# Optimization experiments

Measured on AMD Instinct MI355X. Metric: run time of the kernel, lower is better.

## Reference

```python
import jax, jax.numpy as jnp
import numpy as np

E = 384          # config.n_embd
H = 2 * E        # bidirectional hidden dim
B = 8
T = 128
L = 9            # num_labels


def _lstm_dir(x, w_ih, w_hh, b_ih, b_hh, reverse):
    # x: [B, T, D] -> outputs [B, T, E]
    xs = jnp.swapaxes(x, 0, 1)  # [T, B, D]
    if reverse:
        xs = xs[::-1]
    Eh = w_hh.shape[-1]
    h0 = jnp.zeros((x.shape[0], Eh), x.dtype)

    def step(carry, xt):
        h, c = carry
        g = xt @ w_ih.T + h @ w_hh.T + b_ih + b_hh
        i, f, gg, o = jnp.split(g, 4, axis=-1)
        i = jax.nn.sigmoid(i); f = jax.nn.sigmoid(f)
        gg = jnp.tanh(gg); o = jax.nn.sigmoid(o)
        c = f * c + i * gg
        h = o * jnp.tanh(c)
        return (h, c), h

    _, hs = jax.lax.scan(step, (h0, h0), xs)
    if reverse:
        hs = hs[::-1]
    return jnp.swapaxes(hs, 0, 1)


def bilstm(x, w_ih_l0, w_ih_rest, w_hh, b_ih, b_hh):
    # 3-layer bidirectional LSTM (eval mode: dropout off)
    h = x
    for l in range(3):
        wih = w_ih_l0 if l == 0 else w_ih_rest[l - 1]
        fw = _lstm_dir(h, wih[0], w_hh[l, 0], b_ih[l, 0], b_hh[l, 0], False)
        bw = _lstm_dir(h, wih[1], w_hh[l, 1], b_ih[l, 1], b_hh[l, 1], True)
        h = jnp.concatenate([fw, bw], axis=-1)
    return h  # [B, T, 2E]


def pos_attention(hs, query_ids, W_H, W_p, W_h, v):
    # Vectorized form of the original python loop over target positions.
    shared = hs @ W_H.T                                         # [B,Ts,H] (computed ONCE)
    h_p = jnp.take_along_axis(hs, query_ids[:, :, None].astype(jnp.int32)
                              .repeat(1, axis=1), axis=1)[:, 0, :]  # [B,H]
    p_term = h_p @ W_p.T                                        # [B,H]
    t_term = hs @ W_h.T                                         # [B,Tt,H]
    # score[b,t,s] = v . tanh(shared[b,s] + p_term[b] + t_term[b,t])
    z = jnp.tanh(shared[:, None, :, :] + (p_term[:, None, :] + t_term)[:, :, None, :])
    scores = jnp.einsum('btsh,h->bts', z, v[0])                 # [B,Tt,Ts]
    a = jax.nn.softmax(scores, axis=2)                          # softmax over source dim
    c = jnp.einsum('bts,bsh->bth', a, hs)                       # context [B,Tt,H]
    u = jnp.concatenate([hs, c], axis=-1)                       # [B,Tt,2H]
    at_pool = jnp.mean(a, axis=1)                               # [B,Ts]
    norm = at_pool / jnp.sum(at_pool, axis=1, keepdims=True)
    norm = jnp.nan_to_num(norm, nan=0.0)
    return norm, u


def viterbi_decode(emissions, trans, start, end):
    # emissions: [B,T,L] -> best tag path [B,T]
    score0 = start + emissions[:, 0]                            # [B,L]
    emis_rest = jnp.swapaxes(emissions, 0, 1)[1:]               # [T-1,B,L]

    def step(score, emis_t):
        cand = score[:, :, None] + trans[None]                  # [B,L,L]
        best = jnp.max(cand, axis=1) + emis_t
        ptr = jnp.argmax(cand, axis=1)                          # [B,L]
        return best, ptr

    final, ptrs = jax.lax.scan(step, score0, emis_rest)
    final = final + end
    last = jnp.argmax(final, axis=1)                            # [B]

    def back(tag, ptr_t):
        prev = jnp.take_along_axis(ptr_t, tag[:, None], axis=1)[:, 0]
        return prev, prev

    _, earlier = jax.lax.scan(back, last, ptrs[::-1])           # [T-1,B]
    tags = jnp.concatenate([earlier[::-1], last[None]], axis=0) # [T,B]
    return jnp.swapaxes(tags, 0, 1)                             # [B,T]


def setup_inputs() -> dict:
    key = jax.random.key(0)
    ks = jax.random.split(key, 16)
    s = 0.05
    inp = {}
    inp['input_embeds'] = jax.random.normal(ks[0], (B, T, E), jnp.float32)
    inp['query_ids'] = jax.random.randint(ks[1], (B, 1), 0, T)
    inp['w_ih_l0'] = jax.random.normal(ks[2], (2, 4 * E, E), jnp.float32) * s
    inp['w_ih_rest'] = jax.random.normal(ks[3], (2, 2, 4 * E, 2 * E), jnp.float32) * s
    inp['w_hh'] = jax.random.normal(ks[4], (3, 2, 4 * E, E), jnp.float32) * s
    inp['b_ih'] = jax.random.normal(ks[5], (3, 2, 4 * E), jnp.float32) * s
    inp['b_hh'] = jax.random.normal(ks[6], (3, 2, 4 * E), jnp.float32) * s
    inp['W_H'] = jax.random.normal(ks[7], (H, H), jnp.float32) * s
    inp['W_p'] = jax.random.normal(ks[8], (H, H), jnp.float32) * s
    inp['W_h'] = jax.random.normal(ks[9], (H, H), jnp.float32) * s
    inp['v'] = jax.random.normal(ks[10], (1, H), jnp.float32) * s
    inp['W_clf'] = jax.random.normal(ks[11], (L, 2 * H), jnp.float32) * s
    inp['crf_trans'] = jax.random.normal(ks[12], (L, L), jnp.float32) * s
    inp['crf_start'] = jax.random.normal(ks[13], (L,), jnp.float32) * s
    inp['crf_end'] = jax.random.normal(ks[14], (L,), jnp.float32) * s
    return inp


def reference(input_embeds, query_ids, w_ih_l0, w_ih_rest, w_hh, b_ih, b_hh,
              W_H, W_p, W_h, v, W_clf, crf_trans, crf_start, crf_end):
    hidden_states = bilstm(input_embeds, w_ih_l0, w_ih_rest, w_hh, b_ih, b_hh)
    a_t, u = pos_attention(hidden_states, query_ids, W_H, W_p, W_h, v)
    logits = u @ W_clf.T                                        # [B,T,L]
    tags = viterbi_decode(logits, crf_trans, crf_start, crf_end)
    vit_logits = jnp.where(tags[:, :, None] == jnp.arange(L)[None, None, :], 10, -1).astype(jnp.int8)
    return (vit_logits, hidden_states, a_t)
```

## Files before the change

### kernel.cpp

```cpp
#include <hip/hip_runtime.h>
#include <math.h>

#define Bq 8
#define Tt 128
#define Ee 384
#define Hh 768
#define Ll 9
#define GATE 1536

__device__ __forceinline__ float fast_sigmoid(float x) {
    return 1.f / (1.f + __expf(-x));
}
__device__ __forceinline__ float fast_tanh(float x) {
    return 1.f - 2.f / (__expf(2.f * x) + 1.f);
}

#define BM 64
#define BN 64
#define BKk 16

__global__ __launch_bounds__(256) void k_gemm(
    const float* __restrict__ A, const float* __restrict__ Bw, float* __restrict__ C,
    int M, int N, int K,
    long sAz, long sBz, long sCz,
    const float* __restrict__ b1, const float* __restrict__ b2, long sbz,
    const float* __restrict__ bbn)
{
    int z = blockIdx.z;
    A += (long)z * sAz;
    Bw += (long)z * sBz;
    C += (long)z * sCz;
    const float* bb1 = b1 ? b1 + (long)z * sbz : nullptr;
    const float* bb2 = b2 ? b2 + (long)z * sbz : nullptr;

    int n0 = blockIdx.x * BN;
    int m0 = blockIdx.y * BM;
    int tid = threadIdx.x;

    __shared__ float As[BKk][BM];
    __shared__ float Bs[BKk][BN];

    int lr = tid & 63;
    int lc = (tid >> 6) * 4;
    int tx = tid & 15;
    int ty = tid >> 4;

    float acc[4][4];
#pragma unroll
    for (int i = 0; i < 4; ++i)
#pragma unroll
        for (int j = 0; j < 4; ++j) acc[i][j] = 0.f;

    for (int k0 = 0; k0 < K; k0 += BKk) {
        float4 a0 = *(const float4*)&A[(long)(m0 + lr) * K + k0 + lc];
        float4 w0 = *(const float4*)&Bw[(long)(n0 + lr) * K + k0 + lc];
        __syncthreads();
        As[lc + 0][lr] = a0.x; As[lc + 1][lr] = a0.y; As[lc + 2][lr] = a0.z; As[lc + 3][lr] = a0.w;
        Bs[lc + 0][lr] = w0.x; Bs[lc + 1][lr] = w0.y; Bs[lc + 2][lr] = w0.z; Bs[lc + 3][lr] = w0.w;
        __syncthreads();
#pragma unroll
        for (int kk = 0; kk < BKk; ++kk) {
            float av[4], bv[4];
            *(float4*)&av[0] = *(float4*)&As[kk][ty * 4];
            *(float4*)&bv[0] = *(float4*)&Bs[kk][tx * 4];
#pragma unroll
            for (int i = 0; i < 4; ++i)
#pragma unroll
                for (int j = 0; j < 4; ++j)
                    acc[i][j] = fmaf(av[i], bv[j], acc[i][j]);
        }
    }

#pragma unroll
    for (int i = 0; i < 4; ++i) {
        long m = m0 + ty * 4 + i;
#pragma unroll
        for (int j = 0; j < 4; ++j) {
            int n = n0 + tx * 4 + j;
            float val = acc[i][j];
            if (bb1) val += bb1[n];
            if (bb2) val += bb2[n];
            if (bbn) val += bbn[(m >> 7) * (long)N + n];
            C[m * N + n] = val;
        }
    }
}

__global__ __launch_bounds__(256) void k_gemm2(
    const float* __restrict__ A,
    const float* __restrict__ W0, const float* __restrict__ W1,
    float* __restrict__ C0, float* __restrict__ C1,
    int M, int N, int K,
    const float* __restrict__ bbn)
{
    int z = blockIdx.z;
    const float* Bw = z ? W1 : W0;
    float* C = z ? C1 : C0;
    const float* bb = z ? bbn : nullptr;

    int n0 = blockIdx.x * BN;
    int m0 = blockIdx.y * BM;
    int tid = threadIdx.x;

    __shared__ float As[BKk][BM];
    __shared__ float Bs[BKk][BN];

    int lr = tid & 63;
    int lc = (tid >> 6) * 4;
    int tx = tid & 15;
    int ty = tid >> 4;

    float acc[4][4];
#pragma unroll
    for (int i = 0; i < 4; ++i)
#pragma unroll
        for (int j = 0; j < 4; ++j) acc[i][j] = 0.f;

    for (int k0 = 0; k0 < K; k0 += BKk) {
        float4 a0 = *(const float4*)&A[(long)(m0 + lr) * K + k0 + lc];
        float4 w0 = *(const float4*)&Bw[(long)(n0 + lr) * K + k0 + lc];
        __syncthreads();
        As[lc + 0][lr] = a0.x; As[lc + 1][lr] = a0.y; As[lc + 2][lr] = a0.z; As[lc + 3][lr] = a0.w;
        Bs[lc + 0][lr] = w0.x; Bs[lc + 1][lr] = w0.y; Bs[lc + 2][lr] = w0.z; Bs[lc + 3][lr] = w0.w;
        __syncthreads();
#pragma unroll
        for (int kk = 0; kk < BKk; ++kk) {
            float av[4], bv[4];
            *(float4*)&av[0] = *(float4*)&As[kk][ty * 4];
            *(float4*)&bv[0] = *(float4*)&Bs[kk][tx * 4];
#pragma unroll
            for (int i = 0; i < 4; ++i)
#pragma unroll
                for (int j = 0; j < 4; ++j)
                    acc[i][j] = fmaf(av[i], bv[j], acc[i][j]);
        }
    }

#pragma unroll
    for (int i = 0; i < 4; ++i) {
        long m = m0 + ty * 4 + i;
#pragma unroll
        for (int j = 0; j < 4; ++j) {
            int n = n0 + tx * 4 + j;
            float val = acc[i][j];
            if (bb) val += bb[(m >> 7) * (long)N + n];
            C[m * N + n] = val;
        }
    }
}

__device__ __forceinline__ bool has_sent(unsigned long long v) {
    return ((unsigned)v == 0xFFFFFFFFu) || ((unsigned)(v >> 32) == 0xFFFFFFFFu);
}

__global__ __launch_bounds__(256, 1) void k_lstm(
    const float* __restrict__ G, const float* __restrict__ Whh, float* Yout)
{
    int bid = blockIdx.x;
    int d = bid >> 5;
    int s = bid & 31;
    int tid = threadIdx.x;
    int kq = tid >> 4;
    int rg = tid & 15;
    int kq24 = kq * 24;

    __shared__ float hl[8 * 384];
    __shared__ float part[16 * 392];

    float W_[3][24];
    const float* Wd = Whh + (long)d * GATE * Ee;
#pragma unroll
    for (int r = 0; r < 3; ++r) {
        int rl = rg * 3 + r;
        int g = rl / 12, rr = rl % 12;
        const float* src = Wd + (long)(g * Ee + s * 12 + rr) * Ee + kq24;
#pragma unroll
        for (int k4 = 0; k4 < 6; ++k4) {
            float4 w = *(const float4*)&src[k4 * 4];
            W_[r][k4 * 4 + 0] = w.x;
            W_[r][k4 * 4 + 1] = w.y;
            W_[r][k4 * 4 + 2] = w.z;
            W_[r][k4 * 4 + 3] = w.w;
        }
    }

    float cst = 0.f;
    bool upd = tid < 96;
    int ub = upd ? (tid / 12) : 0;
    int ur = upd ? (tid - ub * 12) : 0;

    float gpre[4];
    const float* gbase = G + ((long)d * 1024 + ub * Tt) * GATE + s * 12 + ur;
    {
        int tt0 = d ? 127 : 0;
        if (upd) {
#pragma unroll
            for (int g = 0; g < 4; ++g) gpre[g] = gbase[(long)tt0 * GATE + g * Ee];
        }
    }

    float4* hl4 = (float4*)hl;

    for (int it = 0; it < 128; ++it) {
        int tt = d ? (127 - it) : it;
        int tp = d ? (tt + 1) : (tt - 1);

        if (it == 0) {
            float4 z4 = make_float4(0.f, 0.f, 0.f, 0.f);
#pragma unroll
            for (int ii = 0; ii < 3; ++ii) hl4[tid + 256 * ii] = z4;
        } else {
            const unsigned long long* sp[6];
            unsigned long long v[6];
#pragma unroll
            for (int ii = 0; ii < 3; ++ii) {
                int i4 = tid + 256 * ii;
                int b = i4 / 96, k4 = i4 - b * 96;
                const unsigned long long* base = (const unsigned long long*)
                    &Yout[((long)(b * Tt + tp)) * Hh + d * Ee + k4 * 4];
                sp[2 * ii] = base;
                sp[2 * ii + 1] = base + 1;
            }
#pragma unroll
            for (int j = 0; j < 6; ++j)
                v[j] = __hip_atomic_load(sp[j], __ATOMIC_RELAXED, __HIP_MEMORY_SCOPE_AGENT);
            for (;;) {
                bool any = false;
#pragma unroll
                for (int j = 0; j < 6; ++j) {
                    if (has_sent(v[j])) {
                        v[j] = __hip_atomic_load(sp[j], __ATOMIC_RELAXED, __HIP_MEMORY_SCOPE_AGENT);
                        any = true;
                    }
                }
                if (!any) break;
            }
#pragma unroll
            for (int ii = 0; ii < 3; ++ii) {
                int i4 = tid + 256 * ii;
                float2 flo = __builtin_bit_cast(float2, v[2 * ii]);
                float2 fhi = __builtin_bit_cast(float2, v[2 * ii + 1]);
                hl4[i4] = make_float4(flo.x, flo.y, fhi.x, fhi.y);
            }
        }
        __syncthreads();

        float acc[8][3];
#pragma unroll
        for (int b = 0; b < 8; ++b)
#pragma unroll
            for (int r = 0; r < 3; ++r) acc[b][r] = 0.f;

#pragma unroll
        for (int k4 = 0; k4 < 6; ++k4) {
#pragma unroll
            for (int b = 0; b < 8; ++b) {
                float4 hv = *(const float4*)&hl[b * 384 + kq24 + k4 * 4];
#pragma unroll
                for (int r = 0; r < 3; ++r) {
                    acc[b][r] = fmaf(W_[r][k4 * 4 + 0], hv.x, acc[b][r]);
                    acc[b][r] = fmaf(W_[r][k4 * 4 + 1], hv.y, acc[b][r]);
                    acc[b][r] = fmaf(W_[r][k4 * 4 + 2], hv.z, acc[b][r]);
                    acc[b][r] = fmaf(W_[r][k4 * 4 + 3], hv.w, acc[b][r]);
                }
            }
        }

#pragma unroll
        for (int b = 0; b < 8; ++b)
#pragma unroll
            for (int r = 0; r < 3; ++r)
                part[kq * 392 + b * 49 + rg * 3 + r] = acc[b][r];
        __syncthreads();

        if (upd) {
            float gt[4];
#pragma unroll
            for (int g = 0; g < 4; ++g) {
                int rl = g * 12 + ur;
                float sum = gpre[g];
#pragma unroll
                for (int q = 0; q < 16; ++q) sum += part[q * 392 + ub * 49 + rl];
                gt[g] = sum;
            }
            float ig = fast_sigmoid(gt[0]);
            float fg = fast_sigmoid(gt[1]);
            float gg = fast_tanh(gt[2]);
            float og = fast_sigmoid(gt[3]);
            cst = fg * cst + ig * gg;
            float h = og * fast_tanh(cst);
            __hip_atomic_store(&Yout[((long)(ub * Tt + tt)) * Hh + d * Ee + s * 12 + ur],
                               h, __ATOMIC_RELAXED, __HIP_MEMORY_SCOPE_AGENT);
            if (it != 127) {
                int ttn = d ? (tt - 1) : (tt + 1);
#pragma unroll
                for (int g = 0; g < 4; ++g) gpre[g] = gbase[(long)ttn * GATE + g * Ee];
            }
        }
    }
}

__global__ void k_fill_sent2(float* __restrict__ a, int na4,
                             float* __restrict__ b, int nb4)
{
    int i = blockIdx.x * 256 + threadIdx.x;
    unsigned u = 0xFFFFFFFFu;
    float f = __builtin_bit_cast(float, u);
    float4 f4 = make_float4(f, f, f, f);
    if (i < na4) ((float4*)a)[i] = f4;
    else {
        int j = i - na4;
        if (j < nb4) ((float4*)b)[j] = f4;
    }
}

__global__ __launch_bounds__(256) void k_pterm(
    const float* __restrict__ hs, const int* __restrict__ qids,
    const float* __restrict__ Wp, float* __restrict__ pterm)
{
    int b = blockIdx.y;
    int chunk = blockIdx.x;
    int tid = threadIdx.x;
    int qid = qids[b];
    __shared__ float hp[Hh];
    for (int i = tid; i < Hh; i += 256) hp[i] = hs[((long)(b * Tt + qid)) * Hh + i];
    __syncthreads();
    int w = tid >> 6, lane = tid & 63;
#pragma unroll
    for (int r = 0; r < 8; ++r) {
        int n = chunk * 32 + w * 8 + r;
        const float* wrow = &Wp[(long)n * Hh];
        float p = 0.f;
#pragma unroll
        for (int k0 = 0; k0 < 3; ++k0) {
            int k = lane * 4 + k0 * 256;
            float4 wv = *(const float4*)&wrow[k];
            float4 hv = *(const float4*)&hp[k];
            p += wv.x * hv.x + wv.y * hv.y + wv.z * hv.z + wv.w * hv.w;
        }
#pragma unroll
        for (int o = 32; o; o >>= 1) p += __shfl_down(p, o);
        if (lane == 0) pterm[b * Hh + n] = p;
    }
}

__global__ __launch_bounds__(256) void k_attn(
    const float* __restrict__ hs, const float* __restrict__ A1, const float* __restrict__ A2,
    const float* __restrict__ v, const float* __restrict__ Wclf,
    float* __restrict__ a_mat, float* __restrict__ logits)
{
    int b = blockIdx.x >> 7, t = blockIdx.x & 127;
    int tid = threadIdx.x;
    long bt = (long)(b * Tt + t);

    __shared__ float a2r[Hh], vr[Hh], hsr[Hh], crow[Hh];
    __shared__ float sc[128], tmp[256], red2[2];

    for (int i = tid; i < Hh; i += 256) {
        a2r[i] = A2[bt * Hh + i];
        vr[i] = v[i];
        hsr[i] = hs[bt * Hh + i];
    }
    __syncthreads();

    {
        int sid = tid >> 1, half = tid & 1;
        float p = 0.f;
        const float* A1r = &A1[((long)(b * Tt + sid)) * Hh + half * 384];
        const float* a2h = &a2r[half * 384];
        const float* vh = &vr[half * 384];
        for (int k = 0; k < 384; k += 4) {
            float4 z = *(const float4*)&A1r[k];
            p += vh[k + 0] * fast_tanh(z.x + a2h[k + 0]);
            p += vh[k + 1] * fast_tanh(z.y + a2h[k + 1]);
            p += vh[k + 2] * fast_tanh(z.z + a2h[k + 2]);
            p += vh[k + 3] * fast_tanh(z.w + a2h[k + 3]);
        }
        tmp[tid] = p;
    }
    __syncthreads();
    if (tid < 128) sc[tid] = tmp[2 * tid] + tmp[2 * tid + 1];
    __syncthreads();

    if (tid < 64) {
        float m = fmaxf(sc[tid], sc[tid + 64]);
#pragma unroll
        for (int o = 32; o; o >>= 1) m = fmaxf(m, __shfl_down(m, o));
        if (tid == 0) red2[0] = m;
    }
    __syncthreads();
    float mx = red2[0];
    if (tid < 128) sc[tid] = __expf(sc[tid] - mx);
    __syncthreads();
    if (tid < 64) {
        float sm = sc[tid] + sc[tid + 64];
#pragma unroll
        for (int o = 32; o; o >>= 1) sm += __shfl_down(sm, o);
        if (tid == 0) red2[1] = sm;
    }
    __syncthreads();
    float inv = 1.f / red2[1];
    if (tid < 128) {
        sc[tid] *= inv;
        a_mat[bt * 128 + tid] = sc[tid];
    }
    __syncthreads();

    float c0 = 0.f, c1 = 0.f, c2 = 0.f;
    for (int s2 = 0; s2 < 128; ++s2) {
        float as = sc[s2];
        const float* hrow = &hs[((long)(b * Tt + s2)) * Hh];
        c0 = fmaf(as, hrow[tid], c0);
        c1 = fmaf(as, hrow[tid + 256], c1);
        c2 = fmaf(as, hrow[tid + 512], c2);
    }
    crow[tid] = c0; crow[tid + 256] = c1; crow[tid + 512] = c2;
    __syncthreads();

    for (int l = 0; l < Ll; ++l) {
        float p = 0.f;
        for (int h = tid; h < 2 * Hh; h += 256) {
            float u = (h < Hh) ? hsr[h] : crow[h - Hh];
            p = fmaf(u, Wclf[l * 2 * Hh + h], p);
        }
#pragma unroll
        for (int o = 32; o; o >>= 1) p += __shfl_down(p, o);
        if ((tid & 63) == 0) tmp[tid >> 6] = p;
        __syncthreads();
        if (tid == 0) logits[bt * Ll + l] = tmp[0] + tmp[1] + tmp[2] + tmp[3];
        __syncthreads();
    }
}

__global__ void k_norm(const float* __restrict__ a_mat, float* __restrict__ a_t)
{
    int b = blockIdx.x;
    int s = threadIdx.x;
    float sum = 0.f;
    for (int t = 0; t < Tt; ++t) sum += a_mat[((long)(b * Tt + t)) * 128 + s];
    __shared__ float pool[128];
    __shared__ float tot;
    pool[s] = sum;
    __syncthreads();
    if (s < 64) {
        float v2 = pool[s] + pool[s + 64];
#pragma unroll
        for (int o = 32; o; o >>= 1) v2 += __shfl_down(v2, o);
        if (s == 0) tot = v2;
    }
    __syncthreads();
    float tv = tot;
    a_t[b * 128 + s] = (tv != 0.f) ? pool[s] / tv : 0.f;
}

__global__ void k_viterbi(const float* __restrict__ logits, const float* __restrict__ trans,
                          const float* __restrict__ start, const float* __restrict__ endw,
                          float* __restrict__ out)
{
    __shared__ float sc[2][72];
    __shared__ unsigned char ptrs[127][72];
    __shared__ unsigned char tags[8][128];
    int tid = threadIdx.x;
    int b = tid / 9, j = tid % 9;
    bool act = tid < 72;
    if (act) sc[0][b * 9 + j] = start[j] + logits[(b * Tt + 0) * Ll + j];
    __syncthreads();
    for (int t = 1; t < Tt; ++t) {
        int cur = t & 1, prv = cur ^ 1;
        if (act) {
            float best = -1e30f; int bi = 0;
#pragma unroll
            for (int i = 0; i < 9; ++i) {
                float vv = sc[prv][b * 9 + i] + trans[i * 9 + j];
                if (vv > best) { best = vv; bi = i; }
            }
            sc[cur][b * 9 + j] = best + logits[(b * Tt + t) * Ll + j];
            ptrs[t - 1][b * 9 + j] = (unsigned char)bi;
        }
        __syncthreads();
    }
    if (act && j == 0) {
        float best = -1e30f; int bj = 0;
#pragma unroll
        for (int jj = 0; jj < 9; ++jj) {
            float vv = sc[1][b * 9 + jj] + endw[jj];
            if (vv > best) { best = vv; bj = jj; }
        }
        int tg = bj;
        tags[b][127] = (unsigned char)tg;
        for (int t = 127; t >= 1; --t) {
            tg = ptrs[t - 1][b * 9 + tg];
            tags[b][t - 1] = (unsigned char)tg;
        }
    }
    __syncthreads();
    for (int i = tid; i < Bq * Tt * Ll; i += blockDim.x) {
        int l = i % 9;
        int btx = i / 9;
        int tt2 = btx % Tt;
        int bb = btx / Tt;
        out[i] = (tags[bb][tt2] == l) ? 10.f : -1.f;
    }
}

extern "C" void kernel_launch(void* const* d_in, const int* in_sizes, int n_in,
                              void* d_out, int out_size, void* d_ws, size_t ws_size,
                              hipStream_t stream)
{
    const float* embeds   = (const float*)d_in[0];
    const int*   qids     = (const int*)d_in[1];
    const float* w_ih_l0  = (const float*)d_in[2];
    const float* w_ih_rest= (const float*)d_in[3];
    const float* w_hh     = (const float*)d_in[4];
    const float* b_ih     = (const float*)d_in[5];
    const float* b_hh     = (const float*)d_in[6];
    const float* W_H      = (const float*)d_in[7];
    const float* W_p      = (const float*)d_in[8];
    const float* W_h      = (const float*)d_in[9];
    const float* vvec     = (const float*)d_in[10];
    const float* W_clf    = (const float*)d_in[11];
    const float* trans    = (const float*)d_in[12];
    const float* cstart   = (const float*)d_in[13];
    const float* cend     = (const float*)d_in[14];

    float* out = (float*)d_out;
    float* vit_out = out;
    float* hs      = out + 9216;
    float* a_t     = out + 9216 + 786432;

    float* ws = (float*)d_ws;
    float* G      = ws;
    float* Y0     = ws + 3145728;
    float* Y1     = Y0 + 786432;
    float* A1     = ws;
    float* A2     = A1 + 786432;
    float* pterm  = A2 + 786432;
    float* a_mat  = pterm + 6144;
    float* logits = a_mat + 131072;

    dim3 blk(256);
    const int nY4 = 2 * 786432 / 4;
    const int nH4 = 786432 / 4;
    const int fillgrid = (nY4 + nH4 + 255) / 256;

    k_fill_sent2<<<dim3(fillgrid), blk, 0, stream>>>(Y0, nY4, hs, nH4);

    k_gemm<<<dim3(GATE / BN, 1024 / BM, 2), blk, 0, stream>>>(
        embeds, w_ih_l0, G, 1024, GATE, Ee,
        0L, (long)GATE * Ee, (long)1024 * GATE,
        b_ih, b_hh, (long)GATE, nullptr);
    k_lstm<<<dim3(64), blk, 0, stream>>>(G, w_hh, Y0);

    k_gemm<<<dim3(GATE / BN, 1024 / BM, 2), blk, 0, stream>>>(
        Y0, w_ih_rest, G, 1024, GATE, Hh,
        0L, (long)GATE * Hh, (long)1024 * GATE,
        b_ih + 2 * GATE, b_hh + 2 * GATE, (long)GATE, nullptr);
    k_lstm<<<dim3(64), blk, 0, stream>>>(G, w_hh + (long)2 * GATE * Ee, Y1);

    k_gemm<<<dim3(GATE / BN, 1024 / BM, 2), blk, 0, stream>>>(
        Y1, w_ih_rest + (long)2 * GATE * Hh, G, 1024, GATE, Hh,
        0L, (long)GATE * Hh, (long)1024 * GATE,
        b_ih + 4 * GATE, b_hh + 4 * GATE, (long)GATE, nullptr);
    k_lstm<<<dim3(64), blk, 0, stream>>>(G, w_hh + (long)4 * GATE * Ee, hs);

    k_pterm<<<dim3(24, 8), blk, 0, stream>>>(hs, qids, W_p, pterm);
    k_gemm2<<<dim3(Hh / BN, 1024 / BM, 2), blk, 0, stream>>>(
        hs, W_H, W_h, A1, A2, 1024, Hh, Hh, pterm);

    k_attn<<<dim3(1024), blk, 0, stream>>>(hs, A1, A2, vvec, W_clf, a_mat, logits);

    k_norm<<<dim3(8), dim3(128), 0, stream>>>(a_mat, a_t);

    k_viterbi<<<dim3(1), dim3(128), 0, stream>>>(logits, trans, cstart, cend, vit_out);
}
```

Baseline: 1.909 ms.

## Overlap LSTM hidden-state polling with matvec and tile attention over 8 targets

In the recurrent LSTM kernel, each thread now polls only the hidden-state slice it consumes and starts accumulating on each chunk as soon as it arrives. This replaces the block-wide gather and barrier before the matvec, removing a __syncthreads from the per-step critical path. The attention kernel now handles 8 target positions per block and stages tiles of A1 in shared memory, so A1, hs and W_clf are reused across targets instead of being reloaded for each one. The trade-offs are much larger shared memory use, a grid that shrinks from 1024 blocks to 128, and a per-thread read pattern in the LSTM that relies on the hl slices lining up with what each thread reads.

```diff
diff --git a/kernel.cpp b/kernel.cpp
--- a/kernel.cpp
+++ b/kernel.cpp
@@ -163,6 +163,8 @@
     int kq = tid >> 4;
     int rg = tid & 15;
     int kq24 = kq * 24;
+    int sb = rg >> 1;
+    int half = rg & 1;
 
     __shared__ float hl[8 * 384];
     __shared__ float part[16 * 392];
@@ -199,69 +201,47 @@
         }
     }
 
-    float4* hl4 = (float4*)hl;
+    unsigned long long* hlu = (unsigned long long*)hl;
+    int lbase = sb * 192 + kq * 12 + half;
 
     for (int it = 0; it < 128; ++it) {
         int tt = d ? (127 - it) : it;
         int tp = d ? (tt + 1) : (tt - 1);
 
+        float acc[8][3];
+#pragma unroll
+        for (int b = 0; b < 8; ++b)
+#pragma unroll
+            for (int r = 0; r < 3; ++r) acc[b][r] = 0.f;
+
         if (it == 0) {
-            float4 z4 = make_float4(0.f, 0.f, 0.f, 0.f);
-#pragma unroll
-            for (int ii = 0; ii < 3; ++ii) hl4[tid + 256 * ii] = z4;
+#pragma unroll
+            for (int m = 0; m < 6; ++m) hlu[lbase + m * 2] = 0ull;
         } else {
+            const unsigned long long* rowbase = (const unsigned long long*)
+                &Yout[((long)(sb * Tt + tp)) * Hh + d * Ee + kq24];
             const unsigned long long* sp[6];
             unsigned long long v[6];
 #pragma unroll
-            for (int ii = 0; ii < 3; ++ii) {
-                int i4 = tid + 256 * ii;
-                int b = i4 / 96, k4 = i4 - b * 96;
-                const unsigned long long* base = (const unsigned long long*)
-                    &Yout[((long)(b * Tt + tp)) * Hh + d * Ee + k4 * 4];
-                sp[2 * ii] = base;
-                sp[2 * ii + 1] = base + 1;
-            }
-#pragma unroll
-            for (int j = 0; j < 6; ++j)
-                v[j] = __hip_atomic_load(sp[j], __ATOMIC_RELAXED, __HIP_MEMORY_SCOPE_AGENT);
-            for (;;) {
-                bool any = false;
-#pragma unroll
-                for (int j = 0; j < 6; ++j) {
-                    if (has_sent(v[j])) {
-                        v[j] = __hip_atomic_load(sp[j], __ATOMIC_RELAXED, __HIP_MEMORY_SCOPE_AGENT);
-                        any = true;
+            for (int m = 0; m < 6; ++m) sp[m] = rowbase + m * 2 + half;
+#pragma unroll
+            for (int m = 0; m < 6; ++m)
+                v[m] = __hip_atomic_load(sp[m], __ATOMIC_RELAXED, __HIP_MEMORY_SCOPE_AGENT);
+#pragma unroll
+            for (int m = 0; m < 6; ++m) {
+                while (has_sent(v[m]))
+                    v[m] = __hip_atomic_load(sp[m], __ATOMIC_RELAXED, __HIP_MEMORY_SCOPE_AGENT);
+                hlu[lbase + m * 2] = v[m];
+#pragma unroll
+                for (int b2 = 0; b2 < 8; ++b2) {
+                    float4 hv = *(const float4*)&hl[b2 * 384 + kq24 + m * 4];
+#pragma unroll
+                    for (int r = 0; r < 3; ++r) {
+                        acc[b2][r] = fmaf(W_[r][m * 4 + 0], hv.x, acc[b2][r]);
+                        acc[b2][r] = fmaf(W_[r][m * 4 + 1], hv.y, acc[b2][r]);
+                        acc[b2][r] = fmaf(W_[r][m * 4 + 2], hv.z, acc[b2][r]);
+                        acc[b2][r] = fmaf(W_[r][m * 4 + 3], hv.w, acc[b2][r]);
                     }
-                }
-                if (!any) break;
-            }
-#pragma unroll
-            for (int ii = 0; ii < 3; ++ii) {
-                int i4 = tid + 256 * ii;
-                float2 flo = __builtin_bit_cast(float2, v[2 * ii]);
-                float2 fhi = __builtin_bit_cast(float2, v[2 * ii + 1]);
-                hl4[i4] = make_float4(flo.x, flo.y, fhi.x, fhi.y);
-            }
-        }
-        __syncthreads();
-
-        float acc[8][3];
-#pragma unroll
-        for (int b = 0; b < 8; ++b)
-#pragma unroll
-            for (int r = 0; r < 3; ++r) acc[b][r] = 0.f;
-
-#pragma unroll
-        for (int k4 = 0; k4 < 6; ++k4) {
-#pragma unroll
-            for (int b = 0; b < 8; ++b) {
-                float4 hv = *(const float4*)&hl[b * 384 + kq24 + k4 * 4];
-#pragma unroll
-                for (int r = 0; r < 3; ++r) {
-                    acc[b][r] = fmaf(W_[r][k4 * 4 + 0], hv.x, acc[b][r]);
-                    acc[b][r] = fmaf(W_[r][k4 * 4 + 1], hv.y, acc[b][r]);
-                    acc[b][r] = fmaf(W_[r][k4 * 4 + 2], hv.z, acc[b][r]);
-                    acc[b][r] = fmaf(W_[r][k4 * 4 + 3], hv.w, acc[b][r]);
                 }
             }
         }
@@ -297,6 +277,7 @@
                 for (int g = 0; g < 4; ++g) gpre[g] = gbase[(long)ttn * GATE + g * Ee];
             }
         }
+        __syncthreads();
     }
 }
 
@@ -349,86 +330,117 @@
     const float* __restrict__ v, const float* __restrict__ Wclf,
     float* __restrict__ a_mat, float* __restrict__ logits)
 {
-    int b = blockIdx.x >> 7, t = blockIdx.x & 127;
+    int b = blockIdx.y;
+    int t0 = blockIdx.x * 8;
     int tid = threadIdx.x;
-    long bt = (long)(b * Tt + t);
-
-    __shared__ float a2r[Hh], vr[Hh], hsr[Hh], crow[Hh];
-    __shared__ float sc[128], tmp[256], red2[2];
-
-    for (int i = tid; i < Hh; i += 256) {
-        a2r[i] = A2[bt * Hh + i];
-        vr[i] = v[i];
-        hsr[i] = hs[bt * Hh + i];
-    }
-    __syncthreads();
+
+    __shared__ float a2r[8][Hh];
+    __shared__ float vr[Hh];
+    __shared__ float a1t[16][769];
+    __shared__ float sc[8][128];
+    __shared__ float hsr[8][Hh];
+    __shared__ float crow[8][Hh];
+
+    for (int i = tid; i < 8 * Hh; i += 256) {
+        int tl = i / Hh, h = i - tl * Hh;
+        a2r[tl][h] = A2[((long)(b * Tt + t0 + tl)) * Hh + h];
+        hsr[tl][h] = hs[((long)(b * Tt + t0 + tl)) * Hh + h];
+    }
+    for (int i = tid; i < Hh; i += 256) vr[i] = v[i];
+    __syncthreads();
+
+    int pr = tid >> 1, shalf = tid & 1;
+    int tl = pr >> 4, sl = pr & 15;
+    for (int st = 0; st < 128; st += 16) {
+        for (int i = tid * 4; i < 16 * Hh; i += 1024) {
+            int r = i / Hh, c = i - r * Hh;
+            float4 x = *(const float4*)&A1[((long)(b * Tt + st + r)) * Hh + c];
+            a1t[r][c] = x.x; a1t[r][c + 1] = x.y; a1t[r][c + 2] = x.z; a1t[r][c + 3] = x.w;
+        }
+        __syncthreads();
+        float p = 0.f;
+        const float* a1p = &a1t[sl][shalf * 384];
+        const float* a2p = &a2r[tl][shalf * 384];
+        const float* vp = &vr[shalf * 384];
+        for (int k = 0; k < 384; k += 4) {
+            p += vp[k + 0] * fast_tanh(a1p[k + 0] + a2p[k + 0]);
+            p += vp[k + 1] * fast_tanh(a1p[k + 1] + a2p[k + 1]);
+            p += vp[k + 2] * fast_tanh(a1p[k + 2] + a2p[k + 2]);
+            p += vp[k + 3] * fast_tanh(a1p[k + 3] + a2p[k + 3]);
+        }
+        p += __shfl_xor(p, 1);
+        if (shalf == 0) sc[tl][st + sl] = p;
+        __syncthreads();
+    }
 
     {
-        int sid = tid >> 1, half = tid & 1;
-        float p = 0.f;
-        const float* A1r = &A1[((long)(b * Tt + sid)) * Hh + half * 384];
-        const float* a2h = &a2r[half * 384];
-        const float* vh = &vr[half * 384];
-        for (int k = 0; k < 384; k += 4) {
-            float4 z = *(const float4*)&A1r[k];
-            p += vh[k + 0] * fast_tanh(z.x + a2h[k + 0]);
-            p += vh[k + 1] * fast_tanh(z.y + a2h[k + 1]);
-            p += vh[k + 2] * fast_tanh(z.z + a2h[k + 2]);
-            p += vh[k + 3] * fast_tanh(z.w + a2h[k + 3]);
-        }
-        tmp[tid] = p;
-    }
-    __syncthreads();
-    if (tid < 128) sc[tid] = tmp[2 * tid] + tmp[2 * tid + 1];
-    __syncthreads();
-
-    if (tid < 64) {
-        float m = fmaxf(sc[tid], sc[tid + 64]);
-#pragma unroll
-        for (int o = 32; o; o >>= 1) m = fmaxf(m, __shfl_down(m, o));
-        if (tid == 0) red2[0] = m;
-    }
-    __syncthreads();
-    float mx = red2[0];
-    if (tid < 128) sc[tid] = __expf(sc[tid] - mx);
-    __syncthreads();
-    if (tid < 64) {
-        float sm = sc[tid] + sc[tid + 64];
-#pragma unroll
-        for (int o = 32; o; o >>= 1) sm += __shfl_down(sm, o);
-        if (tid == 0) red2[1] = sm;
-    }
-    __syncthreads();
-    float inv = 1.f / red2[1];
-    if (tid < 128) {
-        sc[tid] *= inv;
-        a_mat[bt * 128 + tid] = sc[tid];
-    }
-    __syncthreads();
-
-    float c0 = 0.f, c1 = 0.f, c2 = 0.f;
-    for (int s2 = 0; s2 < 128; ++s2) {
-        float as = sc[s2];
-        const float* hrow = &hs[((long)(b * Tt + s2)) * Hh];
-        c0 = fmaf(as, hrow[tid], c0);
-        c1 = fmaf(as, hrow[tid + 256], c1);
-        c2 = fmaf(as, hrow[tid + 512], c2);
-    }
-    crow[tid] = c0; crow[tid + 256] = c1; crow[tid + 512] = c2;
-    __syncthreads();
-
-    for (int l = 0; l < Ll; ++l) {
-        float p = 0.f;
-        for (int h = tid; h < 2 * Hh; h += 256) {
-            float u = (h < Hh) ? hsr[h] : crow[h - Hh];
-            p = fmaf(u, Wclf[l * 2 * Hh + h], p);
-        }
-#pragma unroll
-        for (int o = 32; o; o >>= 1) p += __shfl_down(p, o);
-        if ((tid & 63) == 0) tmp[tid >> 6] = p;
-        __syncthreads();
-        if (tid == 0) logits[bt * Ll + l] = tmp[0] + tmp[1] + tmp[2] + tmp[3];
-        __syncthreads();
+        int g = tid >> 5, l32 = tid & 31;
+        float m = fmaxf(sc[g][l32], fmaxf(sc[g][l32 + 32],
+                 fmaxf(sc[g][l32 + 64], sc[g][l32 + 96])));
+#pragma unroll
+        for (int o = 16; o; o >>= 1) m = fmaxf(m, __shfl_down(m, o, 32));
+        m = __shfl(m, 0, 32);
+        float sm = 0.f;
+#pragma unroll
+        for (int q = 0; q < 4; ++q) {
+            float e = __expf(sc[g][l32 + 32 * q] - m);
+            sc[g][l32 + 32 * q] = e;
+            sm += e;
+        }
+#pragma unroll
+        for (int o = 16; o; o >>= 1) sm += __shfl_down(sm, o, 32);
+        sm = __shfl(sm, 0, 32);
+        float inv = 1.f / sm;
+#pragma unroll
+        for (int q = 0; q < 4; ++q) {
+            float a = sc[g][l32 + 32 * q] * inv;
+            sc[g][l32 + 32 * q] = a;
+            a_mat[((long)(b * Tt + t0 + g)) * 128 + l32 + 32 * q] = a;
+        }
+    }
+    __syncthreads();
+
+    {
+        float ca[8][3];
+#pragma unroll
+        for (int q = 0; q < 8; ++q)
+#pragma unroll
+            for (int c = 0; c < 3; ++c) ca[q][c] = 0.f;
+        int c0 = tid * 3;
+        for (int s2 = 0; s2 < 128; ++s2) {
+            const float* hrow = &hs[((long)(b * Tt + s2)) * Hh + c0];
+            float h0 = hrow[0], h1 = hrow[1], h2 = hrow[2];
+#pragma unroll
+            for (int q = 0; q < 8; ++q) {
+                float a = sc[q][s2];
+                ca[q][0] = fmaf(a, h0, ca[q][0]);
+                ca[q][1] = fmaf(a, h1, ca[q][1]);
+                ca[q][2] = fmaf(a, h2, ca[q][2]);
+            }
+        }
+#pragma unroll
+        for (int q = 0; q < 8; ++q) {
+            crow[q][c0] = ca[q][0];
+            crow[q][c0 + 1] = ca[q][1];
+            crow[q][c0 + 2] = ca[q][2];
+        }
+    }
+    __syncthreads();
+
+    {
+        int w = tid >> 6, l64 = tid & 63;
+        for (int i = w; i < 72; i += 4) {
+            int tl2 = i / 9, l = i - (i / 9) * 9;
+            const float* wr = &Wclf[(long)l * 2 * Hh];
+            float p2 = 0.f;
+            for (int h = l64; h < Hh; h += 64)
+                p2 = fmaf(hsr[tl2][h], wr[h], p2);
+            for (int h = l64; h < Hh; h += 64)
+                p2 = fmaf(crow[tl2][h], wr[Hh + h], p2);
+#pragma unroll
+            for (int o = 32; o; o >>= 1) p2 += __shfl_down(p2, o);
+            if (l64 == 0) logits[((long)(b * Tt + t0 + tl2)) * Ll + l] = p2;
+        }
     }
 }
 
@@ -567,7 +579,7 @@
     k_gemm2<<<dim3(Hh / BN, 1024 / BM, 2), blk, 0, stream>>>(
         hs, W_H, W_h, A1, A2, 1024, Hh, Hh, pterm);
 
-    k_attn<<<dim3(1024), blk, 0, stream>>>(hs, A1, A2, vvec, W_clf, a_mat, logits);
+    k_attn<<<dim3(16, 8), blk, 0, stream>>>(hs, A1, A2, vvec, W_clf, a_mat, logits);
 
     k_norm<<<dim3(8), dim3(128), 0, stream>>>(a_mat, a_t);
 
```

Measured after the change: 2.121 ms. 11.1% more time.
